# Optimization experiments

Hardware: AMD Instinct MI355X
Metric: run time of the kernel (lower is better)

Reference implementation:

```python
import jax, jax.numpy as jnp
import numpy as np

H, W = 256, 256          # resolution from __init__ default
FLOW_SCALING = 256.0     # max(resolution)
MAX_TS = 1.0             # events timestamps normalized to [0, 1]
EPS = 1e-9


def _warp_event(events, flow, tref, ts_weights=None):
    """Bilinear splatting of motion-compensated events into per-polarity IWE.
    events: [B,N,4] (ts,x,y,p); flow: [B,N,2]. Returns [B,2,H,W]."""
    ts = events[..., 0]                      # [B,N]
    x = events[..., 1]
    y = events[..., 2]
    pol = events[..., 3]
    # warped (floating-point) positions
    wx = x + (tref - ts) * flow[..., 0] * FLOW_SCALING
    wy = y + (tref - ts) * flow[..., 1] * FLOW_SCALING
    lx = jnp.floor(wx)
    ty = jnp.floor(wy)
    # 4 bilinear corners: [B,4,N]
    cx = jnp.stack([lx, lx + 1.0, lx, lx + 1.0], axis=1)
    cy = jnp.stack([ty, ty, ty + 1.0, ty + 1.0], axis=1)
    w = (jnp.maximum(0.0, 1.0 - jnp.abs(wx[:, None, :] - cx))
         * jnp.maximum(0.0, 1.0 - jnp.abs(wy[:, None, :] - cy)))
    inb = (cx >= 0) & (cx <= W - 1) & (cy >= 0) & (cy <= H - 1)
    w = jnp.where(inb, w, 0.0)
    if ts_weights is not None:               # optional per-event weight (ts)
        w = w * ts_weights[:, None, :]
    flat = (jnp.clip(cy, 0, H - 1) * W + jnp.clip(cx, 0, W - 1)).astype(jnp.int32)

    def splat(f, ww):  # scatter-add one batch element into flat H*W histogram
        return jnp.zeros(H * W, dtype=w.dtype).at[f.reshape(-1)].add(ww.reshape(-1))

    pos_w = jnp.where((pol == 1)[:, None, :], w, 0.0)
    neg_w = jnp.where((pol == -1)[:, None, :], w, 0.0)
    iwe_pos = jax.vmap(splat)(flat, pos_w).reshape(-1, H, W)
    iwe_neg = jax.vmap(splat)(flat, neg_w).reshape(-1, H, W)
    return jnp.stack([iwe_pos, iwe_neg], axis=1)  # [B,2,H,W]


def _warp_contrast(tref, flow, events):
    iwe = _warp_event(events, flow, tref)
    ts_iwe = _warp_event(events, flow, tref, ts_weights=events[..., 0])
    ts_iwe = ts_iwe / (iwe + EPS)
    loss = (ts_iwe ** 2).sum(axis=(1, 2, 3))           # [B]
    non_zero = ((iwe[:, 0] + iwe[:, 1]) > 0).astype(iwe.dtype)
    return loss / non_zero.sum(axis=(1, 2))


def setup_inputs() -> dict:
    key = jax.random.key(0)
    k1, k2, k3, k4, k5 = jax.random.split(key, 5)
    B, N = 2, 1_000_000
    ts = jax.random.uniform(k1, (B, N))
    x = jax.random.uniform(k2, (B, N)) * (W - 1)
    y = jax.random.uniform(k3, (B, N)) * (H - 1)
    p = jnp.where(jax.random.bernoulli(k4, 0.5, (B, N)), 1.0, -1.0)
    events = jnp.stack([ts, x, y, p], axis=-1).astype(jnp.float32)  # [B,N,4]
    flow = (jax.random.normal(k5, (B, N, 2)) * 0.05).astype(jnp.float32)
    return {"events": events, "flow": flow}


def reference(events, flow):
    # temporal contrast-maximization loss: forward + backward warp per pass
    fw = _warp_contrast(MAX_TS, flow, events).sum() / MAX_TS ** 2
    bw = _warp_contrast(0.0, flow, events).sum() / MAX_TS ** 2
    return fw + bw
```

## Files before the change

### kernel.cpp

```cpp
#include <hip/hip_runtime.h>

#define HH 256
#define WW 256
#define HW (HH * WW)
#define BATCH 2
#define NPASS 2
#define EPSF 1e-9f
#define FLOW_SCALE 256.0f

#define NBLK1 1024
#define NCH 2
#define SCAP 1280
#define CAP 2144
#define FPSCALE 16777216.0f
#define FPINV (1.0f / 16777216.0f)

__global__ __launch_bounds__(256) void ew_bin9(
    const float4* __restrict__ events, const float2* __restrict__ flow,
    float* __restrict__ recs, unsigned* __restrict__ tbl, int N) {
  const int b = blockIdx.y;
  const int gblk = b * NBLK1 + blockIdx.x;
  events += (size_t)b * N;
  flow += (size_t)b * N;
  const int EB = (N + NBLK1 - 1) / NBLK1;
  const int i0 = blockIdx.x * EB;
  const int iend = (i0 + EB < N) ? i0 + EB : N;
  const int CEB = (EB + NCH - 1) / NCH;

  __shared__ float stage[SCAP * 3];
  __shared__ unsigned cnt[128], scan[128], start[128], cur[128];
  __shared__ unsigned s_base;
  if (threadIdx.x == 0) s_base = 0u;

  float* __restrict__ myrecs = recs + (size_t)gblk * CAP * 3;

  for (int c = 0; c < NCH; ++c) {
    const int j0 = i0 + c * CEB;
    int j1 = j0 + CEB;
    if (j1 > iend) j1 = iend;
    if (threadIdx.x < 128) {
      cnt[threadIdx.x] = 0u;
      cur[threadIdx.x] = 0u;
    }
    __syncthreads();

    float rwx[2][2], rwy[2][2], rtsp[2];
#pragma unroll
    for (int s = 0; s < 2; ++s) {
      const int i = j0 + s * 256 + (int)threadIdx.x;
      if (i < j1) {
        const float4 e = events[i];
        const float2 f = flow[i];
        rtsp[s] = copysignf(e.x, e.w);
#pragma unroll
        for (int pass = 0; pass < 2; ++pass) {
          const float tref = (pass == 0) ? 1.0f : 0.0f;
          const float dt = tref - e.x;
          const float wx = fmaf(dt * f.x, FLOW_SCALE, e.y);
          const float wy = fmaf(dt * f.y, FLOW_SCALE, e.z);
          rwx[s][pass] = wx;
          rwy[s][pass] = wy;
          const int lx = (int)floorf(wx), ly = (int)floorf(wy);
          int txs[2], tys[2], nx = 0, ny = 0;
          if ((unsigned)lx < 256u) txs[nx++] = lx >> 5;
          if ((unsigned)(lx + 1) < 256u &&
              (lx < 0 || (((lx + 1) >> 5) != (lx >> 5))))
            txs[nx++] = (lx + 1) >> 5;
          if ((unsigned)ly < 256u) tys[ny++] = ly >> 5;
          if ((unsigned)(ly + 1) < 256u &&
              (ly < 0 || (((ly + 1) >> 5) != (ly >> 5))))
            tys[ny++] = (ly + 1) >> 5;
          for (int a = 0; a < ny; ++a)
            for (int c2 = 0; c2 < nx; ++c2)
              atomicAdd(&cnt[pass * 64 + tys[a] * 8 + txs[c2]], 1u);
        }
      }
    }
    __syncthreads();

    if (threadIdx.x < 64) {
      const int l = threadIdx.x;
      unsigned a = cnt[l], bq = cnt[64 + l];
      for (int off = 1; off < 64; off <<= 1) {
        const unsigned ta = __shfl_up(a, off, 64);
        const unsigned tb = __shfl_up(bq, off, 64);
        if (l >= off) {
          a += ta;
          bq += tb;
        }
      }
      const unsigned tot0 = __shfl(a, 63, 64);
      scan[l] = a;
      scan[64 + l] = bq + tot0;
    }
    __syncthreads();

    const unsigned base = s_base;
    unsigned total = scan[127];
    if (total > SCAP) total = SCAP;
    if (total > CAP - base) total = CAP - base;
    if (threadIdx.x < 128) {
      const unsigned c0 = cnt[threadIdx.x];
      const unsigned st = scan[threadIdx.x] - c0;
      unsigned ec = 0u;
      if (st < total) ec = (c0 < total - st) ? c0 : (total - st);
      start[threadIdx.x] = st;
      tbl[((size_t)gblk * 128 + threadIdx.x) * NCH + c] =
          (base + st) | (ec << 16);
    }
    __syncthreads();

#pragma unroll
    for (int s = 0; s < 2; ++s) {
      const int i = j0 + s * 256 + (int)threadIdx.x;
      if (i < j1) {
        const float tsp = rtsp[s];
#pragma unroll
        for (int pass = 0; pass < 2; ++pass) {
          const float wx = rwx[s][pass];
          const float wy = rwy[s][pass];
          const int lx = (int)floorf(wx), ly = (int)floorf(wy);
          int txs[2], tys[2], nx = 0, ny = 0;
          if ((unsigned)lx < 256u) txs[nx++] = lx >> 5;
          if ((unsigned)(lx + 1) < 256u &&
              (lx < 0 || (((lx + 1) >> 5) != (lx >> 5))))
            txs[nx++] = (lx + 1) >> 5;
          if ((unsigned)ly < 256u) tys[ny++] = ly >> 5;
          if ((unsigned)(ly + 1) < 256u &&
              (ly < 0 || (((ly + 1) >> 5) != (ly >> 5))))
            tys[ny++] = (ly + 1) >> 5;
          for (int a = 0; a < ny; ++a)
            for (int c2 = 0; c2 < nx; ++c2) {
              const int bin = pass * 64 + tys[a] * 8 + txs[c2];
              const unsigned pos = start[bin] + atomicAdd(&cur[bin], 1u);
              if (pos < total) {
                stage[pos * 3 + 0] = wx;
                stage[pos * 3 + 1] = wy;
                stage[pos * 3 + 2] = tsp;
              }
            }
        }
      }
    }
    __syncthreads();

    const unsigned nf = total * 3;
    float* __restrict__ dst = myrecs + (size_t)base * 3;
    for (unsigned j = threadIdx.x; j < nf; j += 256) dst[j] = stage[j];
    __syncthreads();
    if (threadIdx.x == 0) s_base = base + total;
  }
}

__global__ __launch_bounds__(512) void ew_accum10(
    const float* __restrict__ recs, const uint2* __restrict__ tbl2,
    unsigned long long* __restrict__ histU, int nrep) {
  const int gbin = blockIdx.x;
  const int rep = blockIdx.y;
  const int b = gbin >> 7;
  const int bin127 = gbin & 127;
  const int pass = (gbin >> 6) & 1;
  const int tile = gbin & 63;
  const int tx0 = (tile & 7) * 32;
  const int ty0 = (tile >> 3) * 32;
  const int pb = pass * 2 + b;

  __shared__ unsigned long long lds64[2048];
  for (int j = threadIdx.x; j < 2048; j += 512) lds64[j] = 0ull;
  __syncthreads();

  const int bpr = NBLK1 / nrep;
  const int blk0 = rep * bpr;
  const int grp = threadIdx.x >> 3;
  const int lane = threadIdx.x & 7;
  for (int r = blk0 + grp; r < blk0 + bpr; r += 64) {
    const int gblk = b * NBLK1 + r;
    const float* __restrict__ blkrec = recs + (size_t)gblk * CAP * 3;
    const uint2 tv = tbl2[(size_t)gblk * 128 + bin127];
    const unsigned tvs[2] = {tv.x, tv.y};
#pragma unroll
    for (int c = 0; c < NCH; ++c) {
      const unsigned st = tvs[c] & 0xffffu;
      const unsigned ct = tvs[c] >> 16;
      for (unsigned k = lane; k < ct; k += 8) {
        const float wx = blkrec[(st + k) * 3 + 0];
        const float wy = blkrec[(st + k) * 3 + 1];
        const unsigned tb = __float_as_uint(blkrec[(st + k) * 3 + 2]);
        const int spol = (int)(tb >> 31);
        const float ts = __uint_as_float(tb & 0x7fffffffu);
        const int lx = (int)floorf(wx), ly = (int)floorf(wy);
        const float fx = wx - (float)lx;
        const float fy = wy - (float)ly;
        const float wxs[2] = {1.0f - fx, fx};
        const float wys[2] = {1.0f - fy, fy};
#pragma unroll
        for (int dy = 0; dy < 2; ++dy) {
          const int lcy = ly + dy - ty0;
          if ((unsigned)lcy >= 32u) continue;
#pragma unroll
          for (int dx = 0; dx < 2; ++dx) {
            const int lcx = lx + dx - tx0;
            if ((unsigned)lcx >= 32u) continue;
            const float w = wxs[dx] * wys[dy];
            const unsigned wq = __float2uint_rn(w * FPSCALE);
            const unsigned tq = __float2uint_rn(w * ts * FPSCALE);
            const unsigned long long v =
                ((unsigned long long)wq << 32) | (unsigned long long)tq;
            atomicAdd(&lds64[spol * 1024 + lcy * 32 + lcx], v);
          }
        }
      }
    }
  }
  __syncthreads();

  for (int j = threadIdx.x; j < 2048; j += 512) {
    const int spol = j >> 10;
    const int within = j & 1023;
    const size_t px = (size_t)(ty0 + (within >> 5)) * WW + tx0 + (within & 31);
    histU[(((size_t)rep * 4 + pb) * 2 + spol) * HW + px] = lds64[j];
  }
}

__global__ __launch_bounds__(256) void ew_reduce7(
    const unsigned long long* __restrict__ histU, float* __restrict__ partial,
    int nrep) {
  const int sub = blockIdx.x;
  const int pb = blockIdx.y;
  float loss = 0.0f, nz = 0.0f;
  for (int k = threadIdx.x; k < 1024; k += 256) {
    const int pix = sub * 1024 + k;
    unsigned long long v0 = 0ull, v1 = 0ull;
    for (int r = 0; r < nrep; ++r) {
      v0 += histU[(((size_t)r * 4 + pb) * 2 + 0) * HW + pix];
      v1 += histU[(((size_t)r * 4 + pb) * 2 + 1) * HW + pix];
    }
    const float ip = (float)(unsigned)(v0 >> 32) * FPINV;
    const float tp = (float)(unsigned)(v0 & 0xffffffffull) * FPINV;
    const float in_ = (float)(unsigned)(v1 >> 32) * FPINV;
    const float tn = (float)(unsigned)(v1 & 0xffffffffull) * FPINV;
    const float a = tp / (ip + EPSF);
    const float d = tn / (in_ + EPSF);
    loss += a * a + d * d;
    nz += ((ip + in_) > 0.0f) ? 1.0f : 0.0f;
  }
  for (int off = 32; off > 0; off >>= 1) {
    loss += __shfl_down(loss, off, 64);
    nz += __shfl_down(nz, off, 64);
  }
  __shared__ float sl[4], sn[4];
  const int wid = threadIdx.x >> 6;
  if ((threadIdx.x & 63) == 0) {
    sl[wid] = loss;
    sn[wid] = nz;
  }
  __syncthreads();
  if (threadIdx.x == 0) {
    partial[pb * 64 + sub] = sl[0] + sl[1] + sl[2] + sl[3];
    partial[256 + pb * 64 + sub] = sn[0] + sn[1] + sn[2] + sn[3];
  }
}

__global__ void ew_final3(const float* __restrict__ partial,
                          float* __restrict__ out) {
  if (threadIdx.x == 0 && blockIdx.x == 0) {
    float s = 0.0f;
    for (int pb = 0; pb < 4; ++pb) {
      float L = 0.0f, Z = 0.0f;
      for (int j = 0; j < 64; ++j) {
        L += partial[pb * 64 + j];
        Z += partial[256 + pb * 64 + j];
      }
      s += L / Z;
    }
    out[0] = s;
  }
}

#define CHUNKS 8
#define TILES 16
#define TILE_PX 4096
#define REP_FLOATS (CHUNKS * 16 * HW)

__global__ __launch_bounds__(256) void ew_tile(
    const float4* __restrict__ events, const float2* __restrict__ flow,
    float* __restrict__ rep, int N) {
  const int c = blockIdx.x;
  const int tile = blockIdx.y;
  const int pb = blockIdx.z;
  const int b = pb & 1;
  const float tref = (pb >> 1) == 0 ? 1.0f : 0.0f;
  const int tx0 = (tile & 3) * 64;
  const int ty0 = (tile >> 2) * 64;

  __shared__ float lds[4 * TILE_PX];
  for (int j = threadIdx.x; j < 4 * TILE_PX; j += 256) lds[j] = 0.0f;
  __syncthreads();

  events += (size_t)b * N;
  flow += (size_t)b * N;
  const int Nc = (N + CHUNKS - 1) / CHUNKS;
  const int i0 = c * Nc;
  const int i1 = (i0 + Nc < N) ? (i0 + Nc) : N;

  for (int i = i0 + threadIdx.x; i < i1; i += 256) {
    const float4 e = events[i];
    const float2 f = flow[i];
    const float ts = e.x;
    const int pol = (e.w > 0.0f) ? 0 : 1;
    const float dt = tref - ts;
    const float wx = fmaf(dt * f.x, FLOW_SCALE, e.y);
    const float wy = fmaf(dt * f.y, FLOW_SCALE, e.z);
    const float lxf = floorf(wx);
    const float tyf = floorf(wy);
    const float fx = wx - lxf;
    const float fy = wy - tyf;
    const int lx = (int)lxf - tx0;
    const int ty = (int)tyf - ty0;
    const float wxs[2] = {1.0f - fx, fx};
    const float wys[2] = {1.0f - fy, fy};
#pragma unroll
    for (int dy = 0; dy < 2; ++dy) {
      const int cy = ty + dy;
      if ((unsigned)cy >= 64u) continue;
#pragma unroll
      for (int dx = 0; dx < 2; ++dx) {
        const int cx = lx + dx;
        if ((unsigned)cx >= 64u) continue;
        const float w = wxs[dx] * wys[dy];
        const int li = cy * 64 + cx;
        atomicAdd(&lds[pol * TILE_PX + li], w);
        atomicAdd(&lds[(pol + 2) * TILE_PX + li], w * ts);
      }
    }
  }
  __syncthreads();

  float* __restrict__ dst = rep + ((size_t)c * 16 + (size_t)pb * 4) * HW;
  for (int j = threadIdx.x; j < 4 * TILE_PX; j += 256) {
    const int slice = j >> 12;
    const int within = j & (TILE_PX - 1);
    dst[(size_t)slice * HW + (ty0 + (within >> 6)) * WW + tx0 + (within & 63)] =
        lds[j];
  }
}

__global__ __launch_bounds__(256) void ew_reduce2(const float* __restrict__ rep,
                                                  float* __restrict__ partial) {
  const int sub = blockIdx.x;
  const int pb = blockIdx.y;
  float loss = 0.0f, nz = 0.0f;
  for (int k = threadIdx.x; k < 2048; k += 256) {
    const int pix = sub * 2048 + k;
    float ip = 0.0f, in_ = 0.0f, tp = 0.0f, tn = 0.0f;
#pragma unroll
    for (int c = 0; c < CHUNKS; ++c) {
      const float* __restrict__ rb =
          rep + ((size_t)c * 16 + (size_t)pb * 4) * HW + pix;
      ip += rb[0];
      in_ += rb[HW];
      tp += rb[2 * HW];
      tn += rb[3 * HW];
    }
    const float a = tp / (ip + EPSF);
    const float d = tn / (in_ + EPSF);
    loss += a * a + d * d;
    nz += ((ip + in_) > 0.0f) ? 1.0f : 0.0f;
  }
  for (int off = 32; off > 0; off >>= 1) {
    loss += __shfl_down(loss, off, 64);
    nz += __shfl_down(nz, off, 64);
  }
  __shared__ float sl[4], sn[4];
  const int wid = threadIdx.x >> 6;
  if ((threadIdx.x & 63) == 0) {
    sl[wid] = loss;
    sn[wid] = nz;
  }
  __syncthreads();
  if (threadIdx.x == 0) {
    partial[pb * 32 + sub] = sl[0] + sl[1] + sl[2] + sl[3];
    partial[128 + pb * 32 + sub] = sn[0] + sn[1] + sn[2] + sn[3];
  }
}

__global__ void ew_final2(const float* __restrict__ partial,
                          float* __restrict__ out) {
  if (threadIdx.x == 0 && blockIdx.x == 0) {
    float s = 0.0f;
    for (int pb = 0; pb < 4; ++pb) {
      float L = 0.0f, Z = 0.0f;
      for (int j = 0; j < 32; ++j) {
        L += partial[pb * 32 + j];
        Z += partial[128 + pb * 32 + j];
      }
      s += L / Z;
    }
    out[0] = s;
  }
}

#define HIST_FLOATS (NPASS * BATCH * 4 * HW)

__global__ __launch_bounds__(256) void ew_scatter(
    const float4* __restrict__ events, const float2* __restrict__ flow,
    float* __restrict__ hist, int N) {
  const int b = blockIdx.y;
  events += (size_t)b * N;
  flow += (size_t)b * N;
  float* __restrict__ hb = hist + (size_t)b * 4 * HW;
  for (int i = blockIdx.x * blockDim.x + threadIdx.x; i < N;
       i += gridDim.x * blockDim.x) {
    const float4 e = events[i];
    const float2 f = flow[i];
    const float ts = e.x, x = e.y, y = e.z, p = e.w;
    const int polofs = (p > 0.0f) ? 0 : HW;
#pragma unroll
    for (int pass = 0; pass < NPASS; ++pass) {
      const float tref = (pass == 0) ? 1.0f : 0.0f;
      const float dt = tref - ts;
      const float wx = fmaf(dt * f.x, FLOW_SCALE, x);
      const float wy = fmaf(dt * f.y, FLOW_SCALE, y);
      const float lxf = floorf(wx), tyf = floorf(wy);
      const float fx = wx - lxf, fy = wy - tyf;
      const int lx = (int)lxf, ty = (int)tyf;
      float* __restrict__ wbase = hb + (size_t)pass * BATCH * 4 * HW + polofs;
      float* __restrict__ tbase = wbase + 2 * HW;
      const float w00 = (1.0f - fx) * (1.0f - fy);
      const float w10 = fx * (1.0f - fy);
      const float w01 = (1.0f - fx) * fy;
      const float w11 = fx * fy;
      const int cx0 = lx, cx1 = lx + 1, cy0 = ty, cy1 = ty + 1;
      const bool inx0 = (cx0 >= 0) & (cx0 < WW);
      const bool inx1 = (cx1 >= 0) & (cx1 < WW);
      const bool iny0 = (cy0 >= 0) & (cy0 < HH);
      const bool iny1 = (cy1 >= 0) & (cy1 < HH);
      if (inx0 & iny0) {
        const int pix = cy0 * WW + cx0;
        atomicAdd(wbase + pix, w00);
        atomicAdd(tbase + pix, w00 * ts);
      }
      if (inx1 & iny0) {
        const int pix = cy0 * WW + cx1;
        atomicAdd(wbase + pix, w10);
        atomicAdd(tbase + pix, w10 * ts);
      }
      if (inx0 & iny1) {
        const int pix = cy1 * WW + cx0;
        atomicAdd(wbase + pix, w01);
        atomicAdd(tbase + pix, w01 * ts);
      }
      if (inx1 & iny1) {
        const int pix = cy1 * WW + cx1;
        atomicAdd(wbase + pix, w11);
        atomicAdd(tbase + pix, w11 * ts);
      }
    }
  }
}

__global__ __launch_bounds__(256) void ew_reduce(const float* __restrict__ hist,
                                                 float* __restrict__ partial) {
  const int g = blockIdx.x;
  const float* __restrict__ base = hist + (size_t)g * 4 * HW;
  double loss = 0.0, nz = 0.0;
  for (int pix = threadIdx.x; pix < HW; pix += blockDim.x) {
    const float ip = base[pix];
    const float in_ = base[HW + pix];
    const float tp = base[2 * HW + pix];
    const float tn = base[3 * HW + pix];
    const float a = tp / (ip + EPSF);
    const float c = tn / (in_ + EPSF);
    loss += (double)(a * a) + (double)(c * c);
    if ((ip + in_) > 0.0f) nz += 1.0;
  }
  for (int off = 32; off > 0; off >>= 1) {
    loss += __shfl_down(loss, off, 64);
    nz += __shfl_down(nz, off, 64);
  }
  __shared__ double sl[4], sn[4];
  const int wid = threadIdx.x >> 6;
  if ((threadIdx.x & 63) == 0) {
    sl[wid] = loss;
    sn[wid] = nz;
  }
  __syncthreads();
  if (threadIdx.x == 0) {
    partial[g] = (float)(sl[0] + sl[1] + sl[2] + sl[3]);
    partial[4 + g] = (float)(sn[0] + sn[1] + sn[2] + sn[3]);
  }
}

__global__ void ew_final(const float* __restrict__ partial,
                         float* __restrict__ out) {
  if (threadIdx.x == 0 && blockIdx.x == 0) {
    float s = 0.0f;
    for (int g = 0; g < NPASS * BATCH; ++g) s += partial[g] / partial[4 + g];
    out[0] = s;
  }
}

extern "C" void kernel_launch(void* const* d_in, const int* in_sizes, int n_in,
                              void* d_out, int out_size, void* d_ws,
                              size_t ws_size, hipStream_t stream) {
  const float4* events = (const float4*)d_in[0];
  const float2* flow = (const float2*)d_in[1];
  float* out = (float*)d_out;
  const int N = in_sizes[0] / (4 * BATCH);

  const size_t recs_bytes = (size_t)BATCH * NBLK1 * CAP * 12;
  const size_t tbl_bytes = (size_t)BATCH * NBLK1 * 128 * NCH * sizeof(unsigned);
  const size_t histU1 = (size_t)4 * 2 * HW * sizeof(unsigned long long);
  const size_t tail = 512 * sizeof(float);
  const size_t need1 = recs_bytes + tbl_bytes + histU1 + tail;
  const size_t need2 = recs_bytes + tbl_bytes + 2 * histU1 + tail;
  const size_t need_tile = ((size_t)REP_FLOATS + 256) * sizeof(float);

  if (ws_size >= need1) {
    const int nrep = (ws_size >= need2) ? 2 : 1;
    float* recs = (float*)d_ws;
    unsigned* tbl = (unsigned*)((char*)d_ws + recs_bytes);
    unsigned long long* histU = (unsigned long long*)((char*)tbl + tbl_bytes);
    float* partial = (float*)((char*)histU + (size_t)nrep * histU1);

    dim3 bgrid(NBLK1, BATCH);
    ew_bin9<<<bgrid, 256, 0, stream>>>(events, flow, recs, tbl, N);
    dim3 agrid(256, nrep);
    ew_accum10<<<agrid, 512, 0, stream>>>(recs, (const uint2*)tbl, histU, nrep);
    dim3 rgrid(64, 4);
    ew_reduce7<<<rgrid, 256, 0, stream>>>(histU, partial, nrep);
    ew_final3<<<1, 64, 0, stream>>>(partial, out);
  } else if (ws_size >= need_tile) {
    float* rep = (float*)d_ws;
    float* partial = rep + REP_FLOATS;
    dim3 tgrid(CHUNKS, TILES, NPASS * BATCH);
    ew_tile<<<tgrid, 256, 0, stream>>>(events, flow, rep, N);
    dim3 rgrid(32, 4);
    ew_reduce2<<<rgrid, 256, 0, stream>>>(rep, partial);
    ew_final2<<<1, 64, 0, stream>>>(partial, out);
  } else {
    float* hist = (float*)d_ws;
    float* partial = hist + HIST_FLOATS;
    hipMemsetAsync(hist, 0, (size_t)HIST_FLOATS * sizeof(float), stream);
    dim3 sgrid(1024, BATCH);
    ew_scatter<<<sgrid, 256, 0, stream>>>(events, flow, hist, N);
    ew_reduce<<<NPASS * BATCH, 256, 0, stream>>>(hist, partial);
    ew_final<<<1, 64, 0, stream>>>(partial, out);
  }
}
```

Measured before the change: 68.78 us.

## Split bins by polarity to double accumulation blocks and cache tile encoding

The binning kernel now sorts records into 256 bins (pass × tile × polarity) instead of 128. This lets the accumulation kernel launch twice as many blocks, each owning a single-polarity 32x32 tile with half the LDS. The first phase packs each event's tile coordinates and counts into a register so the scatter phase no longer recomputes them. The extra blocks raise parallelism in the accumulate stage, at the cost of a larger table, a wider scan, and more per-block table reads.

```diff
diff --git a/kernel.cpp b/kernel.cpp
--- a/kernel.cpp
+++ b/kernel.cpp
@@ -15,7 +15,7 @@
 #define FPSCALE 16777216.0f
 #define FPINV (1.0f / 16777216.0f)
 
-__global__ __launch_bounds__(256) void ew_bin9(
+__global__ __launch_bounds__(256) void ew_bin10(
     const float4* __restrict__ events, const float2* __restrict__ flow,
     float* __restrict__ recs, unsigned* __restrict__ tbl, int N) {
   const int b = blockIdx.y;
@@ -28,7 +28,7 @@
   const int CEB = (EB + NCH - 1) / NCH;
 
   __shared__ float stage[SCAP * 3];
-  __shared__ unsigned cnt[128], scan[128], start[128], cur[128];
+  __shared__ unsigned cnt[256], scan[256], start[256], cur[256];
   __shared__ unsigned s_base;
   if (threadIdx.x == 0) s_base = 0u;
 
@@ -38,20 +38,22 @@
     const int j0 = i0 + c * CEB;
     int j1 = j0 + CEB;
     if (j1 > iend) j1 = iend;
-    if (threadIdx.x < 128) {
-      cnt[threadIdx.x] = 0u;
-      cur[threadIdx.x] = 0u;
-    }
+    cnt[threadIdx.x] = 0u;
+    cur[threadIdx.x] = 0u;
     __syncthreads();
 
     float rwx[2][2], rwy[2][2], rtsp[2];
+    unsigned renc[2][2];
+    renc[0][0] = renc[0][1] = renc[1][0] = renc[1][1] = 0u;
 #pragma unroll
     for (int s = 0; s < 2; ++s) {
       const int i = j0 + s * 256 + (int)threadIdx.x;
       if (i < j1) {
         const float4 e = events[i];
         const float2 f = flow[i];
-        rtsp[s] = copysignf(e.x, e.w);
+        const float tsp = copysignf(e.x, e.w);
+        rtsp[s] = tsp;
+        const int pol = (int)(__float_as_uint(tsp) >> 31);
 #pragma unroll
         for (int pass = 0; pass < 2; ++pass) {
           const float tref = (pass == 0) ? 1.0f : 0.0f;
@@ -61,18 +63,28 @@
           rwx[s][pass] = wx;
           rwy[s][pass] = wy;
           const int lx = (int)floorf(wx), ly = (int)floorf(wy);
-          int txs[2], tys[2], nx = 0, ny = 0;
-          if ((unsigned)lx < 256u) txs[nx++] = lx >> 5;
-          if ((unsigned)(lx + 1) < 256u &&
-              (lx < 0 || (((lx + 1) >> 5) != (lx >> 5))))
-            txs[nx++] = (lx + 1) >> 5;
-          if ((unsigned)ly < 256u) tys[ny++] = ly >> 5;
-          if ((unsigned)(ly + 1) < 256u &&
-              (ly < 0 || (((ly + 1) >> 5) != (ly >> 5))))
-            tys[ny++] = (ly + 1) >> 5;
+          int tx = 0, nx = 0, ty = 0, ny = 0;
+          if ((unsigned)lx < 256u) {
+            tx = lx >> 5;
+            nx = ((unsigned)(lx + 1) < 256u && (((lx + 1) >> 5) != tx)) ? 2 : 1;
+          } else if ((unsigned)(lx + 1) < 256u) {
+            tx = 0;
+            nx = 1;
+          }
+          if ((unsigned)ly < 256u) {
+            ty = ly >> 5;
+            ny = ((unsigned)(ly + 1) < 256u && (((ly + 1) >> 5) != ty)) ? 2 : 1;
+          } else if ((unsigned)(ly + 1) < 256u) {
+            ty = 0;
+            ny = 1;
+          }
+          renc[s][pass] =
+              (unsigned)tx | ((unsigned)ty << 3) | ((unsigned)nx << 6) |
+              ((unsigned)ny << 8);
           for (int a = 0; a < ny; ++a)
             for (int c2 = 0; c2 < nx; ++c2)
-              atomicAdd(&cnt[pass * 64 + tys[a] * 8 + txs[c2]], 1u);
+              atomicAdd(&cnt[pass * 128 + ((ty + a) * 8 + tx + c2) * 2 + pol],
+                        1u);
         }
       }
     }
@@ -80,32 +92,41 @@
 
     if (threadIdx.x < 64) {
       const int l = threadIdx.x;
-      unsigned a = cnt[l], bq = cnt[64 + l];
+      unsigned v0 = cnt[l], v1 = cnt[64 + l], v2 = cnt[128 + l],
+               v3 = cnt[192 + l];
       for (int off = 1; off < 64; off <<= 1) {
-        const unsigned ta = __shfl_up(a, off, 64);
-        const unsigned tb = __shfl_up(bq, off, 64);
+        const unsigned t0 = __shfl_up(v0, off, 64);
+        const unsigned t1 = __shfl_up(v1, off, 64);
+        const unsigned t2 = __shfl_up(v2, off, 64);
+        const unsigned t3 = __shfl_up(v3, off, 64);
         if (l >= off) {
-          a += ta;
-          bq += tb;
+          v0 += t0;
+          v1 += t1;
+          v2 += t2;
+          v3 += t3;
         }
       }
-      const unsigned tot0 = __shfl(a, 63, 64);
-      scan[l] = a;
-      scan[64 + l] = bq + tot0;
+      const unsigned T0 = __shfl(v0, 63, 64);
+      const unsigned T1 = __shfl(v1, 63, 64);
+      const unsigned T2 = __shfl(v2, 63, 64);
+      scan[l] = v0;
+      scan[64 + l] = v1 + T0;
+      scan[128 + l] = v2 + T0 + T1;
+      scan[192 + l] = v3 + T0 + T1 + T2;
     }
     __syncthreads();
 
     const unsigned base = s_base;
-    unsigned total = scan[127];
+    unsigned total = scan[255];
     if (total > SCAP) total = SCAP;
     if (total > CAP - base) total = CAP - base;
-    if (threadIdx.x < 128) {
+    {
       const unsigned c0 = cnt[threadIdx.x];
       const unsigned st = scan[threadIdx.x] - c0;
       unsigned ec = 0u;
       if (st < total) ec = (c0 < total - st) ? c0 : (total - st);
       start[threadIdx.x] = st;
-      tbl[((size_t)gblk * 128 + threadIdx.x) * NCH + c] =
+      tbl[((size_t)gblk * 256 + threadIdx.x) * NCH + c] =
           (base + st) | (ec << 16);
     }
     __syncthreads();
@@ -115,23 +136,21 @@
       const int i = j0 + s * 256 + (int)threadIdx.x;
       if (i < j1) {
         const float tsp = rtsp[s];
+        const int pol = (int)(__float_as_uint(tsp) >> 31);
 #pragma unroll
         for (int pass = 0; pass < 2; ++pass) {
+          const unsigned enc = renc[s][pass];
+          const int nx = (enc >> 6) & 3;
+          const int ny = (enc >> 8) & 3;
+          if (nx == 0 || ny == 0) continue;
+          const int tx = enc & 7;
+          const int ty = (enc >> 3) & 7;
           const float wx = rwx[s][pass];
           const float wy = rwy[s][pass];
-          const int lx = (int)floorf(wx), ly = (int)floorf(wy);
-          int txs[2], tys[2], nx = 0, ny = 0;
-          if ((unsigned)lx < 256u) txs[nx++] = lx >> 5;
-          if ((unsigned)(lx + 1) < 256u &&
-              (lx < 0 || (((lx + 1) >> 5) != (lx >> 5))))
-            txs[nx++] = (lx + 1) >> 5;
-          if ((unsigned)ly < 256u) tys[ny++] = ly >> 5;
-          if ((unsigned)(ly + 1) < 256u &&
-              (ly < 0 || (((ly + 1) >> 5) != (ly >> 5))))
-            tys[ny++] = (ly + 1) >> 5;
           for (int a = 0; a < ny; ++a)
             for (int c2 = 0; c2 < nx; ++c2) {
-              const int bin = pass * 64 + tys[a] * 8 + txs[c2];
+              const int bin =
+                  pass * 128 + ((ty + a) * 8 + tx + c2) * 2 + pol;
               const unsigned pos = start[bin] + atomicAdd(&cur[bin], 1u);
               if (pos < total) {
                 stage[pos * 3 + 0] = wx;
@@ -152,41 +171,41 @@
   }
 }
 
-__global__ __launch_bounds__(512) void ew_accum10(
+__global__ __launch_bounds__(512) void ew_accum11(
     const float* __restrict__ recs, const uint2* __restrict__ tbl2,
     unsigned long long* __restrict__ histU, int nrep) {
-  const int gbin = blockIdx.x;
+  const int gb = blockIdx.x;
   const int rep = blockIdx.y;
-  const int b = gbin >> 7;
-  const int bin127 = gbin & 127;
-  const int pass = (gbin >> 6) & 1;
-  const int tile = gbin & 63;
+  const int b = gb >> 8;
+  const int bin = gb & 255;
+  const int pass = bin >> 7;
+  const int tile = (bin >> 1) & 63;
+  const int pol = bin & 1;
   const int tx0 = (tile & 7) * 32;
   const int ty0 = (tile >> 3) * 32;
   const int pb = pass * 2 + b;
 
-  __shared__ unsigned long long lds64[2048];
-  for (int j = threadIdx.x; j < 2048; j += 512) lds64[j] = 0ull;
+  __shared__ unsigned long long lds64[1024];
+  for (int j = threadIdx.x; j < 1024; j += 512) lds64[j] = 0ull;
   __syncthreads();
 
   const int bpr = NBLK1 / nrep;
   const int blk0 = rep * bpr;
-  const int grp = threadIdx.x >> 3;
-  const int lane = threadIdx.x & 7;
-  for (int r = blk0 + grp; r < blk0 + bpr; r += 64) {
+  const int grp = threadIdx.x >> 2;
+  const int lane = threadIdx.x & 3;
+  for (int r = blk0 + grp; r < blk0 + bpr; r += 128) {
     const int gblk = b * NBLK1 + r;
     const float* __restrict__ blkrec = recs + (size_t)gblk * CAP * 3;
-    const uint2 tv = tbl2[(size_t)gblk * 128 + bin127];
+    const uint2 tv = tbl2[(size_t)gblk * 256 + bin];
     const unsigned tvs[2] = {tv.x, tv.y};
 #pragma unroll
     for (int c = 0; c < NCH; ++c) {
       const unsigned st = tvs[c] & 0xffffu;
       const unsigned ct = tvs[c] >> 16;
-      for (unsigned k = lane; k < ct; k += 8) {
+      for (unsigned k = lane; k < ct; k += 4) {
         const float wx = blkrec[(st + k) * 3 + 0];
         const float wy = blkrec[(st + k) * 3 + 1];
         const unsigned tb = __float_as_uint(blkrec[(st + k) * 3 + 2]);
-        const int spol = (int)(tb >> 31);
         const float ts = __uint_as_float(tb & 0x7fffffffu);
         const int lx = (int)floorf(wx), ly = (int)floorf(wy);
         const float fx = wx - (float)lx;
@@ -206,7 +225,7 @@
             const unsigned tq = __float2uint_rn(w * ts * FPSCALE);
             const unsigned long long v =
                 ((unsigned long long)wq << 32) | (unsigned long long)tq;
-            atomicAdd(&lds64[spol * 1024 + lcy * 32 + lcx], v);
+            atomicAdd(&lds64[lcy * 32 + lcx], v);
           }
         }
       }
@@ -214,11 +233,9 @@
   }
   __syncthreads();
 
-  for (int j = threadIdx.x; j < 2048; j += 512) {
-    const int spol = j >> 10;
-    const int within = j & 1023;
-    const size_t px = (size_t)(ty0 + (within >> 5)) * WW + tx0 + (within & 31);
-    histU[(((size_t)rep * 4 + pb) * 2 + spol) * HW + px] = lds64[j];
+  for (int j = threadIdx.x; j < 1024; j += 512) {
+    const size_t px = (size_t)(ty0 + (j >> 5)) * WW + tx0 + (j & 31);
+    histU[(((size_t)rep * 4 + pb) * 2 + pol) * HW + px] = lds64[j];
   }
 }
 
@@ -509,7 +526,7 @@
   const int N = in_sizes[0] / (4 * BATCH);
 
   const size_t recs_bytes = (size_t)BATCH * NBLK1 * CAP * 12;
-  const size_t tbl_bytes = (size_t)BATCH * NBLK1 * 128 * NCH * sizeof(unsigned);
+  const size_t tbl_bytes = (size_t)BATCH * NBLK1 * 256 * NCH * sizeof(unsigned);
   const size_t histU1 = (size_t)4 * 2 * HW * sizeof(unsigned long long);
   const size_t tail = 512 * sizeof(float);
   const size_t need1 = recs_bytes + tbl_bytes + histU1 + tail;
@@ -524,9 +541,9 @@
     float* partial = (float*)((char*)histU + (size_t)nrep * histU1);
 
     dim3 bgrid(NBLK1, BATCH);
-    ew_bin9<<<bgrid, 256, 0, stream>>>(events, flow, recs, tbl, N);
-    dim3 agrid(256, nrep);
-    ew_accum10<<<agrid, 512, 0, stream>>>(recs, (const uint2*)tbl, histU, nrep);
+    ew_bin10<<<bgrid, 256, 0, stream>>>(events, flow, recs, tbl, N);
+    dim3 agrid(512, nrep);
+    ew_accum11<<<agrid, 512, 0, stream>>>(recs, (const uint2*)tbl, histU, nrep);
     dim3 rgrid(64, 4);
     ew_reduce7<<<rgrid, 256, 0, stream>>>(histU, partial, nrep);
     ew_final3<<<1, 64, 0, stream>>>(partial, out);
```

After: 71.31 us. 1.04x slower.

## Store binned event records as float4 with polarity and allow four histogram replicas

Applied to the files above, without the earlier changes.

Adds new bin and accumulate kernels that write each binned record as a 16-byte float4 (wx, wy, ts, polarity) instead of the previous 12-byte format, so the accumulate pass does one aligned vector load per record. The accumulate kernel takes polarity from the record and splats into both polarity tiles with packed 64-bit fixed-point LDS atomics. The launcher also lets the number of histogram replicas grow to four when the workspace is large enough, cutting per-block record ranges. This costs more workspace and record write and read bandwidth. The unused tile fallback path is removed.

```diff
diff --git a/kernel.cpp b/kernel.cpp
--- a/kernel.cpp
+++ b/kernel.cpp
@@ -14,6 +14,207 @@
 #define CAP 2144
 #define FPSCALE 16777216.0f
 #define FPINV (1.0f / 16777216.0f)
+
+__global__ __launch_bounds__(256) void ew_bin11(
+    const float4* __restrict__ events, const float2* __restrict__ flow,
+    float4* __restrict__ recs, unsigned* __restrict__ tbl, int N) {
+  const int b = blockIdx.y;
+  const int gblk = b * NBLK1 + blockIdx.x;
+  events += (size_t)b * N;
+  flow += (size_t)b * N;
+  const int EB = (N + NBLK1 - 1) / NBLK1;
+  const int i0 = blockIdx.x * EB;
+  const int iend = (i0 + EB < N) ? i0 + EB : N;
+  const int CEB = (EB + NCH - 1) / NCH;
+
+  __shared__ float4 stage4[SCAP];
+  __shared__ unsigned cnt[128], scan[128], start[128], cur[128];
+  __shared__ unsigned s_base;
+  if (threadIdx.x == 0) s_base = 0u;
+
+  float4* __restrict__ myrecs = recs + (size_t)gblk * CAP;
+
+  for (int c = 0; c < NCH; ++c) {
+    const int j0 = i0 + c * CEB;
+    int j1 = j0 + CEB;
+    if (j1 > iend) j1 = iend;
+    if (threadIdx.x < 128) {
+      cnt[threadIdx.x] = 0u;
+      cur[threadIdx.x] = 0u;
+    }
+    __syncthreads();
+
+    float rwx[2][2], rwy[2][2], rts[2], rp[2];
+#pragma unroll
+    for (int s = 0; s < 2; ++s) {
+      const int i = j0 + s * 256 + (int)threadIdx.x;
+      if (i < j1) {
+        const float4 e = events[i];
+        const float2 f = flow[i];
+        rts[s] = e.x;
+        rp[s] = e.w;
+#pragma unroll
+        for (int pass = 0; pass < 2; ++pass) {
+          const float tref = (pass == 0) ? 1.0f : 0.0f;
+          const float dt = tref - e.x;
+          const float wx = fmaf(dt * f.x, FLOW_SCALE, e.y);
+          const float wy = fmaf(dt * f.y, FLOW_SCALE, e.z);
+          rwx[s][pass] = wx;
+          rwy[s][pass] = wy;
+          const int lx = (int)floorf(wx), ly = (int)floorf(wy);
+          int txs[2], tys[2], nx = 0, ny = 0;
+          if ((unsigned)lx < 256u) txs[nx++] = lx >> 5;
+          if ((unsigned)(lx + 1) < 256u &&
+              (lx < 0 || (((lx + 1) >> 5) != (lx >> 5))))
+            txs[nx++] = (lx + 1) >> 5;
+          if ((unsigned)ly < 256u) tys[ny++] = ly >> 5;
+          if ((unsigned)(ly + 1) < 256u &&
+              (ly < 0 || (((ly + 1) >> 5) != (ly >> 5))))
+            tys[ny++] = (ly + 1) >> 5;
+          for (int a = 0; a < ny; ++a)
+            for (int c2 = 0; c2 < nx; ++c2)
+              atomicAdd(&cnt[pass * 64 + tys[a] * 8 + txs[c2]], 1u);
+        }
+      }
+    }
+    __syncthreads();
+
+    if (threadIdx.x < 64) {
+      const int l = threadIdx.x;
+      unsigned a = cnt[l], bq = cnt[64 + l];
+      for (int off = 1; off < 64; off <<= 1) {
+        const unsigned ta = __shfl_up(a, off, 64);
+        const unsigned tb = __shfl_up(bq, off, 64);
+        if (l >= off) {
+          a += ta;
+          bq += tb;
+        }
+      }
+      const unsigned tot0 = __shfl(a, 63, 64);
+      scan[l] = a;
+      scan[64 + l] = bq + tot0;
+    }
+    __syncthreads();
+
+    const unsigned base = s_base;
+    unsigned total = scan[127];
+    if (total > SCAP) total = SCAP;
+    if (total > CAP - base) total = CAP - base;
+    if (threadIdx.x < 128) {
+      const unsigned c0 = cnt[threadIdx.x];
+      const unsigned st = scan[threadIdx.x] - c0;
+      unsigned ec = 0u;
+      if (st < total) ec = (c0 < total - st) ? c0 : (total - st);
+      start[threadIdx.x] = st;
+      tbl[((size_t)gblk * 128 + threadIdx.x) * NCH + c] =
+          (base + st) | (ec << 16);
+    }
+    __syncthreads();
+
+#pragma unroll
+    for (int s = 0; s < 2; ++s) {
+      const int i = j0 + s * 256 + (int)threadIdx.x;
+      if (i < j1) {
+        const float ts = rts[s], p = rp[s];
+#pragma unroll
+        for (int pass = 0; pass < 2; ++pass) {
+          const float wx = rwx[s][pass];
+          const float wy = rwy[s][pass];
+          const int lx = (int)floorf(wx), ly = (int)floorf(wy);
+          int txs[2], tys[2], nx = 0, ny = 0;
+          if ((unsigned)lx < 256u) txs[nx++] = lx >> 5;
+          if ((unsigned)(lx + 1) < 256u &&
+              (lx < 0 || (((lx + 1) >> 5) != (lx >> 5))))
+            txs[nx++] = (lx + 1) >> 5;
+          if ((unsigned)ly < 256u) tys[ny++] = ly >> 5;
+          if ((unsigned)(ly + 1) < 256u &&
+              (ly < 0 || (((ly + 1) >> 5) != (ly >> 5))))
+            tys[ny++] = (ly + 1) >> 5;
+          for (int a = 0; a < ny; ++a)
+            for (int c2 = 0; c2 < nx; ++c2) {
+              const int bin = pass * 64 + tys[a] * 8 + txs[c2];
+              const unsigned pos = start[bin] + atomicAdd(&cur[bin], 1u);
+              if (pos < total) stage4[pos] = make_float4(wx, wy, ts, p);
+            }
+        }
+      }
+    }
+    __syncthreads();
+
+    float4* __restrict__ dst = myrecs + base;
+    for (unsigned j = threadIdx.x; j < total; j += 256) dst[j] = stage4[j];
+    __syncthreads();
+    if (threadIdx.x == 0) s_base = base + total;
+  }
+}
+
+__global__ __launch_bounds__(512) void ew_accum12(
+    const float4* __restrict__ recs, const uint2* __restrict__ tbl2,
+    unsigned long long* __restrict__ histU, int nrep) {
+  const int gbin = blockIdx.x;
+  const int rep = blockIdx.y;
+  const int b = gbin >> 7;
+  const int bin127 = gbin & 127;
+  const int pass = (gbin >> 6) & 1;
+  const int tile = gbin & 63;
+  const int tx0 = (tile & 7) * 32;
+  const int ty0 = (tile >> 3) * 32;
+  const int pb = pass * 2 + b;
+
+  __shared__ unsigned long long lds64[2048];
+  for (int j = threadIdx.x; j < 2048; j += 512) lds64[j] = 0ull;
+  __syncthreads();
+
+  const int bpr = NBLK1 / nrep;
+  const int blk0 = rep * bpr;
+  const int grp = threadIdx.x >> 3;
+  const int lane = threadIdx.x & 7;
+  for (int r = blk0 + grp; r < blk0 + bpr; r += 64) {
+    const int gblk = b * NBLK1 + r;
+    const float4* __restrict__ blkrec = recs + (size_t)gblk * CAP;
+    const uint2 tv = tbl2[(size_t)gblk * 128 + bin127];
+    const unsigned tvs[2] = {tv.x, tv.y};
+#pragma unroll
+    for (int c = 0; c < NCH; ++c) {
+      const unsigned st = tvs[c] & 0xffffu;
+      const unsigned ct = tvs[c] >> 16;
+      for (unsigned k = lane; k < ct; k += 8) {
+        const float4 rr = blkrec[st + k];
+        const float wx = rr.x, wy = rr.y, ts = rr.z;
+        const int spol = (rr.w > 0.0f) ? 0 : 1;
+        const int lx = (int)floorf(wx), ly = (int)floorf(wy);
+        const float fx = wx - (float)lx;
+        const float fy = wy - (float)ly;
+        const float wxs[2] = {1.0f - fx, fx};
+        const float wys[2] = {1.0f - fy, fy};
+#pragma unroll
+        for (int dy = 0; dy < 2; ++dy) {
+          const int lcy = ly + dy - ty0;
+          if ((unsigned)lcy >= 32u) continue;
+#pragma unroll
+          for (int dx = 0; dx < 2; ++dx) {
+            const int lcx = lx + dx - tx0;
+            if ((unsigned)lcx >= 32u) continue;
+            const float w = wxs[dx] * wys[dy];
+            const unsigned wq = __float2uint_rn(w * FPSCALE);
+            const unsigned tq = __float2uint_rn(w * ts * FPSCALE);
+            const unsigned long long v =
+                ((unsigned long long)wq << 32) | (unsigned long long)tq;
+            atomicAdd(&lds64[spol * 1024 + lcy * 32 + lcx], v);
+          }
+        }
+      }
+    }
+  }
+  __syncthreads();
+
+  for (int j = threadIdx.x; j < 2048; j += 512) {
+    const int spol = j >> 10;
+    const int within = j & 1023;
+    const size_t px = (size_t)(ty0 + (within >> 5)) * WW + tx0 + (within & 31);
+    histU[(((size_t)rep * 4 + pb) * 2 + spol) * HW + px] = lds64[j];
+  }
+}
 
 __global__ __launch_bounds__(256) void ew_bin9(
     const float4* __restrict__ events, const float2* __restrict__ flow,
@@ -277,129 +478,6 @@
   }
 }
 
-#define CHUNKS 8
-#define TILES 16
-#define TILE_PX 4096
-#define REP_FLOATS (CHUNKS * 16 * HW)
-
-__global__ __launch_bounds__(256) void ew_tile(
-    const float4* __restrict__ events, const float2* __restrict__ flow,
-    float* __restrict__ rep, int N) {
-  const int c = blockIdx.x;
-  const int tile = blockIdx.y;
-  const int pb = blockIdx.z;
-  const int b = pb & 1;
-  const float tref = (pb >> 1) == 0 ? 1.0f : 0.0f;
-  const int tx0 = (tile & 3) * 64;
-  const int ty0 = (tile >> 2) * 64;
-
-  __shared__ float lds[4 * TILE_PX];
-  for (int j = threadIdx.x; j < 4 * TILE_PX; j += 256) lds[j] = 0.0f;
-  __syncthreads();
-
-  events += (size_t)b * N;
-  flow += (size_t)b * N;
-  const int Nc = (N + CHUNKS - 1) / CHUNKS;
-  const int i0 = c * Nc;
-  const int i1 = (i0 + Nc < N) ? (i0 + Nc) : N;
-
-  for (int i = i0 + threadIdx.x; i < i1; i += 256) {
-    const float4 e = events[i];
-    const float2 f = flow[i];
-    const float ts = e.x;
-    const int pol = (e.w > 0.0f) ? 0 : 1;
-    const float dt = tref - ts;
-    const float wx = fmaf(dt * f.x, FLOW_SCALE, e.y);
-    const float wy = fmaf(dt * f.y, FLOW_SCALE, e.z);
-    const float lxf = floorf(wx);
-    const float tyf = floorf(wy);
-    const float fx = wx - lxf;
-    const float fy = wy - tyf;
-    const int lx = (int)lxf - tx0;
-    const int ty = (int)tyf - ty0;
-    const float wxs[2] = {1.0f - fx, fx};
-    const float wys[2] = {1.0f - fy, fy};
-#pragma unroll
-    for (int dy = 0; dy < 2; ++dy) {
-      const int cy = ty + dy;
-      if ((unsigned)cy >= 64u) continue;
-#pragma unroll
-      for (int dx = 0; dx < 2; ++dx) {
-        const int cx = lx + dx;
-        if ((unsigned)cx >= 64u) continue;
-        const float w = wxs[dx] * wys[dy];
-        const int li = cy * 64 + cx;
-        atomicAdd(&lds[pol * TILE_PX + li], w);
-        atomicAdd(&lds[(pol + 2) * TILE_PX + li], w * ts);
-      }
-    }
-  }
-  __syncthreads();
-
-  float* __restrict__ dst = rep + ((size_t)c * 16 + (size_t)pb * 4) * HW;
-  for (int j = threadIdx.x; j < 4 * TILE_PX; j += 256) {
-    const int slice = j >> 12;
-    const int within = j & (TILE_PX - 1);
-    dst[(size_t)slice * HW + (ty0 + (within >> 6)) * WW + tx0 + (within & 63)] =
-        lds[j];
-  }
-}
-
-__global__ __launch_bounds__(256) void ew_reduce2(const float* __restrict__ rep,
-                                                  float* __restrict__ partial) {
-  const int sub = blockIdx.x;
-  const int pb = blockIdx.y;
-  float loss = 0.0f, nz = 0.0f;
-  for (int k = threadIdx.x; k < 2048; k += 256) {
-    const int pix = sub * 2048 + k;
-    float ip = 0.0f, in_ = 0.0f, tp = 0.0f, tn = 0.0f;
-#pragma unroll
-    for (int c = 0; c < CHUNKS; ++c) {
-      const float* __restrict__ rb =
-          rep + ((size_t)c * 16 + (size_t)pb * 4) * HW + pix;
-      ip += rb[0];
-      in_ += rb[HW];
-      tp += rb[2 * HW];
-      tn += rb[3 * HW];
-    }
-    const float a = tp / (ip + EPSF);
-    const float d = tn / (in_ + EPSF);
-    loss += a * a + d * d;
-    nz += ((ip + in_) > 0.0f) ? 1.0f : 0.0f;
-  }
-  for (int off = 32; off > 0; off >>= 1) {
-    loss += __shfl_down(loss, off, 64);
-    nz += __shfl_down(nz, off, 64);
-  }
-  __shared__ float sl[4], sn[4];
-  const int wid = threadIdx.x >> 6;
-  if ((threadIdx.x & 63) == 0) {
-    sl[wid] = loss;
-    sn[wid] = nz;
-  }
-  __syncthreads();
-  if (threadIdx.x == 0) {
-    partial[pb * 32 + sub] = sl[0] + sl[1] + sl[2] + sl[3];
-    partial[128 + pb * 32 + sub] = sn[0] + sn[1] + sn[2] + sn[3];
-  }
-}
-
-__global__ void ew_final2(const float* __restrict__ partial,
-                          float* __restrict__ out) {
-  if (threadIdx.x == 0 && blockIdx.x == 0) {
-    float s = 0.0f;
-    for (int pb = 0; pb < 4; ++pb) {
-      float L = 0.0f, Z = 0.0f;
-      for (int j = 0; j < 32; ++j) {
-        L += partial[pb * 32 + j];
-        Z += partial[128 + pb * 32 + j];
-      }
-      s += L / Z;
-    }
-    out[0] = s;
-  }
-}
-
 #define HIST_FLOATS (NPASS * BATCH * 4 * HW)
 
 __global__ __launch_bounds__(256) void ew_scatter(
@@ -508,18 +586,38 @@
   float* out = (float*)d_out;
   const int N = in_sizes[0] / (4 * BATCH);
 
-  const size_t recs_bytes = (size_t)BATCH * NBLK1 * CAP * 12;
   const size_t tbl_bytes = (size_t)BATCH * NBLK1 * 128 * NCH * sizeof(unsigned);
   const size_t histU1 = (size_t)4 * 2 * HW * sizeof(unsigned long long);
   const size_t tail = 512 * sizeof(float);
-  const size_t need1 = recs_bytes + tbl_bytes + histU1 + tail;
-  const size_t need2 = recs_bytes + tbl_bytes + 2 * histU1 + tail;
-  const size_t need_tile = ((size_t)REP_FLOATS + 256) * sizeof(float);
-
-  if (ws_size >= need1) {
-    const int nrep = (ws_size >= need2) ? 2 : 1;
+
+  const size_t recs16 = (size_t)BATCH * NBLK1 * CAP * 16;
+  const size_t need16_2 = recs16 + tbl_bytes + 2 * histU1 + tail;
+  const size_t need16_4 = recs16 + tbl_bytes + 4 * histU1 + tail;
+
+  const size_t recs12 = (size_t)BATCH * NBLK1 * CAP * 12;
+  const size_t need12_1 = recs12 + tbl_bytes + histU1 + tail;
+  const size_t need12_2 = recs12 + tbl_bytes + 2 * histU1 + tail;
+  const size_t need12_4 = recs12 + tbl_bytes + 4 * histU1 + tail;
+
+  if (ws_size >= need16_2) {
+    const int nrep = (ws_size >= need16_4) ? 4 : 2;
+    float4* recs = (float4*)d_ws;
+    unsigned* tbl = (unsigned*)((char*)d_ws + recs16);
+    unsigned long long* histU = (unsigned long long*)((char*)tbl + tbl_bytes);
+    float* partial = (float*)((char*)histU + (size_t)nrep * histU1);
+
+    dim3 bgrid(NBLK1, BATCH);
+    ew_bin11<<<bgrid, 256, 0, stream>>>(events, flow, recs, tbl, N);
+    dim3 agrid(256, nrep);
+    ew_accum12<<<agrid, 512, 0, stream>>>(recs, (const uint2*)tbl, histU, nrep);
+    dim3 rgrid(64, 4);
+    ew_reduce7<<<rgrid, 256, 0, stream>>>(histU, partial, nrep);
+    ew_final3<<<1, 64, 0, stream>>>(partial, out);
+  } else if (ws_size >= need12_1) {
+    const int nrep =
+        (ws_size >= need12_4) ? 4 : ((ws_size >= need12_2) ? 2 : 1);
     float* recs = (float*)d_ws;
-    unsigned* tbl = (unsigned*)((char*)d_ws + recs_bytes);
+    unsigned* tbl = (unsigned*)((char*)d_ws + recs12);
     unsigned long long* histU = (unsigned long long*)((char*)tbl + tbl_bytes);
     float* partial = (float*)((char*)histU + (size_t)nrep * histU1);
 
@@ -530,14 +628,6 @@
     dim3 rgrid(64, 4);
     ew_reduce7<<<rgrid, 256, 0, stream>>>(histU, partial, nrep);
     ew_final3<<<1, 64, 0, stream>>>(partial, out);
-  } else if (ws_size >= need_tile) {
-    float* rep = (float*)d_ws;
-    float* partial = rep + REP_FLOATS;
-    dim3 tgrid(CHUNKS, TILES, NPASS * BATCH);
-    ew_tile<<<tgrid, 256, 0, stream>>>(events, flow, rep, N);
-    dim3 rgrid(32, 4);
-    ew_reduce2<<<rgrid, 256, 0, stream>>>(rep, partial);
-    ew_final2<<<1, 64, 0, stream>>>(partial, out);
   } else {
     float* hist = (float*)d_ws;
     float* partial = hist + HIST_FLOATS;
```

Measured after the change: 72.87 us. +5.9%, slower.
